# Kernel tuning notes

Hardware: AMD Instinct MI355X
Metric: run time of the kernel (lower is better)

## Reference

```python
import jax, jax.numpy as jnp
import numpy as np

DELTA_V = 0.5
DELTA_D = 1.5
ALPHA = 1.0
BETA = 1.0
GAMMA = 0.001
K = 33  # label ids 0..32; 0 = background (ignored)
EPS = 1e-12


def setup_inputs() -> dict:
    key = jax.random.key(0)
    k1, k2 = jax.random.split(key)
    B, N, E = 8, 65536, 32
    embeddings = jax.random.normal(k1, (B, N, E), dtype=jnp.float32)
    labels = jax.random.randint(k2, (B, N), 0, K)
    return {"embeddings": embeddings, "labels": labels}


def reference(embeddings, labels):
    B, N, E = embeddings.shape
    dt = embeddings.dtype
    seg = (labels + jnp.arange(B)[:, None] * K).reshape(-1)  # (B*N,)

    # segment mean -> per-instance centers (B, K, E)
    sums = jax.ops.segment_sum(embeddings.reshape(B * N, E), seg, num_segments=B * K).reshape(B, K, E)
    counts = jax.ops.segment_sum(jnp.ones((B * N,), dtype=dt), seg, num_segments=B * K).reshape(B, K)
    centers = sums / jnp.maximum(counts, 1.0)[..., None]

    present = counts > 0
    present = present.at[:, 0].set(False)  # drop background label 0
    presf = present.astype(dt)
    n_inst = presf.sum(axis=1)  # (B,)

    # ---- variance term: per-point hinge distance to own center, segment-mean ----
    c_per_point = centers[jnp.arange(B)[:, None], labels]  # (B, N, E) gather
    d2 = ((embeddings - c_per_point) ** 2).sum(-1)
    dist = jnp.sqrt(jnp.maximum(d2, EPS))
    hinge = jnp.where(labels > 0, jnp.maximum(dist - DELTA_V, 0.0), 0.0)
    per_inst_sum = jax.ops.segment_sum(hinge.reshape(-1), seg, num_segments=B * K).reshape(B, K)
    per_inst_mean = per_inst_sum / jnp.maximum(counts, 1.0)
    variance_term = (per_inst_mean * presf).sum(1) / jnp.maximum(n_inst, 1.0)

    # ---- distance term: pairwise hinge between present instance centers ----
    diff2 = ((centers[:, :, None, :] - centers[:, None, :, :]) ** 2).sum(-1)  # (B,K,K)
    upper = jnp.triu(jnp.ones((K, K), dtype=bool), 1)[None]
    pair_valid = present[:, :, None] & present[:, None, :] & upper
    cd = jnp.sqrt(jnp.maximum(jnp.where(pair_valid, diff2, 1.0), EPS))
    pair_hinge = jnp.maximum(2.0 * DELTA_D - cd, 0.0) * pair_valid.astype(dt)
    n_pairs = n_inst * (n_inst - 1.0) * 0.5
    distance_term = pair_hinge.sum((1, 2)) / jnp.maximum(n_pairs, 1.0)

    # ---- regularization: mean L2 norm of present centers ----
    c_norm = jnp.sqrt(jnp.maximum((centers ** 2).sum(-1), EPS))
    reg_term = (c_norm * presf).sum(1) / jnp.maximum(n_inst, 1.0)

    per_batch = ALPHA * variance_term + BETA * distance_term + GAMMA * reg_term
    per_batch = jnp.where(n_inst > 0, per_batch, 0.0)
    return per_batch.sum() / B
```

## Files before the change

### kernel.cpp

```cpp
#include <hip/hip_runtime.h>
#include <math.h>

#define KC 33
#define ED 32
#define KE (KC * ED)
#define PAD 33

#define BPB_A 64
#define TPA 128
#define NSLOT 8
#define BPB_H 128
#define TPH 256


__global__ void k_zero(float* __restrict__ ws, int n, float* __restrict__ out) {
    int i = blockIdx.x * blockDim.x + threadIdx.x;
    if (i < n) ws[i] = 0.f;
    if (i == 0) out[0] = 0.f;
}

__global__ __launch_bounds__(256) void k_hist(const int* __restrict__ lab,
                                              float* __restrict__ counts, int N) {
    __shared__ float h[4 * KC];
    int t = threadIdx.x;
    int w = t >> 6;
    if (t < 4 * KC) h[t] = 0.f;
    __syncthreads();
    int b   = blockIdx.x >> 5;
    int blk = blockIdx.x & 31;
    const int4* l4 = (const int4*)(lab + (size_t)b * N + (size_t)blk * 2048);
    int4 a = l4[t];
    int4 c = l4[t + 256];
    float* hw = &h[w * KC];
    atomicAdd(&hw[a.x], 1.f); atomicAdd(&hw[a.y], 1.f);
    atomicAdd(&hw[a.z], 1.f); atomicAdd(&hw[a.w], 1.f);
    atomicAdd(&hw[c.x], 1.f); atomicAdd(&hw[c.y], 1.f);
    atomicAdd(&hw[c.z], 1.f); atomicAdd(&hw[c.w], 1.f);
    __syncthreads();
    if (t < KC)
        atomicAdd(&counts[b * KC + t], h[t] + h[KC + t] + h[2 * KC + t] + h[3 * KC + t]);
}

__global__ __launch_bounds__(256) void k_accum(const float* __restrict__ emb,
                                               const int* __restrict__ lab,
                                               float* __restrict__ sums, int N) {
    __shared__ float s_tile[TPA * PAD];
    __shared__ float s_priv[NSLOT * KE];
    __shared__ int   s_lab[TPA];
    int t = threadIdx.x;
    for (int i = t; i < NSLOT * KE; i += 256) s_priv[i] = 0.f;

    int b     = blockIdx.x / BPB_A;
    int blk   = blockIdx.x % BPB_A;
    int chunk = N / BPB_A;
    int e     = t & 31;
    int slot  = t >> 5;
    size_t pbase = (size_t)b * N + (size_t)blk * chunk;
    const int NT = chunk / TPA;

    const float4* g4 = (const float4*)(emb + pbase * ED);
    float4 r0 = g4[t], r1 = g4[t + 256], r2 = g4[t + 512], r3 = g4[t + 768];
    int rl = 0;
    if (t < TPA) rl = lab[pbase + t];
    __syncthreads();

    for (int tb = 0; tb < NT; tb++) {
        {
            int f, p, m;
            f = t;        p = f >> 3; m = (f & 7) * 4;
            { float* d = &s_tile[PAD * p + m]; d[0]=r0.x; d[1]=r0.y; d[2]=r0.z; d[3]=r0.w; }
            f = t + 256;  p = f >> 3; m = (f & 7) * 4;
            { float* d = &s_tile[PAD * p + m]; d[0]=r1.x; d[1]=r1.y; d[2]=r1.z; d[3]=r1.w; }
            f = t + 512;  p = f >> 3; m = (f & 7) * 4;
            { float* d = &s_tile[PAD * p + m]; d[0]=r2.x; d[1]=r2.y; d[2]=r2.z; d[3]=r2.w; }
            f = t + 768;  p = f >> 3; m = (f & 7) * 4;
            { float* d = &s_tile[PAD * p + m]; d[0]=r3.x; d[1]=r3.y; d[2]=r3.z; d[3]=r3.w; }
        }
        if (t < TPA) s_lab[t] = rl;
        __syncthreads();

        if (tb + 1 < NT) {
            const float4* gn = (const float4*)(emb + (pbase + (size_t)(tb + 1) * TPA) * ED);
            r0 = gn[t]; r1 = gn[t + 256]; r2 = gn[t + 512]; r3 = gn[t + 768];
            if (t < TPA) rl = lab[pbase + (size_t)(tb + 1) * TPA + t];
        }

        float* priv = &s_priv[slot * KE];
#pragma unroll
        for (int st = 0; st < TPA / NSLOT; st++) {
            int pt = st * NSLOT + slot;
            float x = s_tile[pt * PAD + e];
            int   k = s_lab[pt];
            priv[k * ED + e] += x;
        }
        __syncthreads();
    }

    for (int i = t; i < KE; i += 256) {
        float v = 0.f;
#pragma unroll
        for (int s = 0; s < NSLOT; s++) v += s_priv[s * KE + i];
        atomicAdd(&sums[(size_t)b * KE + i], v);
    }
}

__global__ __launch_bounds__(256) void k_hinge(const float* __restrict__ emb,
                                               const int* __restrict__ lab,
                                               const float* __restrict__ sums,
                                               const float* __restrict__ counts,
                                               float* __restrict__ var, int N) {
    __shared__ float s_tile[TPH * PAD];
    __shared__ float s_ctr[KC * PAD];
    __shared__ float s_cnt[KC];
    __shared__ float s_inv[KC];
    __shared__ int   s_lab[TPH];
    __shared__ float s_red[4];
    int t     = threadIdx.x;
    int b     = blockIdx.x / BPB_H;
    int blk   = blockIdx.x % BPB_H;
    int chunk = N / BPB_H;
    size_t pbase = (size_t)b * N + (size_t)blk * chunk;
    const int NT = chunk / TPH;

    const float4* g4 = (const float4*)(emb + pbase * ED);
    float4 r0 = g4[t],        r1 = g4[t + 256],  r2 = g4[t + 512],  r3 = g4[t + 768];
    float4 r4 = g4[t + 1024], r5 = g4[t + 1280], r6 = g4[t + 1536], r7 = g4[t + 1792];
    int rl = lab[pbase + t];

    if (t < KC) {
        float c = counts[b * KC + t];
        s_cnt[t] = fmaxf(c, 1.f);
        s_inv[t] = (t > 0 && c > 0.f) ? 1.f / fmaxf(c, 1.f) : 0.f;
    }
    __syncthreads();
    for (int i = t; i < KE; i += 256) {
        int k = i >> 5, e = i & 31;
        s_ctr[k * PAD + e] = sums[(size_t)b * KE + i] / s_cnt[k];
    }

    float hs = 0.f;
    for (int tb = 0; tb < NT; tb++) {
        {
            int f, p, m;
            f = t;         p = f >> 3; m = (f & 7) * 4;
            { float* d = &s_tile[PAD * p + m]; d[0]=r0.x; d[1]=r0.y; d[2]=r0.z; d[3]=r0.w; }
            f = t + 256;   p = f >> 3; m = (f & 7) * 4;
            { float* d = &s_tile[PAD * p + m]; d[0]=r1.x; d[1]=r1.y; d[2]=r1.z; d[3]=r1.w; }
            f = t + 512;   p = f >> 3; m = (f & 7) * 4;
            { float* d = &s_tile[PAD * p + m]; d[0]=r2.x; d[1]=r2.y; d[2]=r2.z; d[3]=r2.w; }
            f = t + 768;   p = f >> 3; m = (f & 7) * 4;
            { float* d = &s_tile[PAD * p + m]; d[0]=r3.x; d[1]=r3.y; d[2]=r3.z; d[3]=r3.w; }
            f = t + 1024;  p = f >> 3; m = (f & 7) * 4;
            { float* d = &s_tile[PAD * p + m]; d[0]=r4.x; d[1]=r4.y; d[2]=r4.z; d[3]=r4.w; }
            f = t + 1280;  p = f >> 3; m = (f & 7) * 4;
            { float* d = &s_tile[PAD * p + m]; d[0]=r5.x; d[1]=r5.y; d[2]=r5.z; d[3]=r5.w; }
            f = t + 1536;  p = f >> 3; m = (f & 7) * 4;
            { float* d = &s_tile[PAD * p + m]; d[0]=r6.x; d[1]=r6.y; d[2]=r6.z; d[3]=r6.w; }
            f = t + 1792;  p = f >> 3; m = (f & 7) * 4;
            { float* d = &s_tile[PAD * p + m]; d[0]=r7.x; d[1]=r7.y; d[2]=r7.z; d[3]=r7.w; }
        }
        s_lab[t] = rl;
        __syncthreads();

        if (tb + 1 < NT) {
            const float4* gn = (const float4*)(emb + (pbase + (size_t)(tb + 1) * TPH) * ED);
            r0 = gn[t];        r1 = gn[t + 256];  r2 = gn[t + 512];  r3 = gn[t + 768];
            r4 = gn[t + 1024]; r5 = gn[t + 1280]; r6 = gn[t + 1536]; r7 = gn[t + 1792];
            rl = lab[pbase + (size_t)(tb + 1) * TPH + t];
        }

        int   k  = s_lab[t];
        float iv = s_inv[k];
        const float* xr = &s_tile[t * PAD];
        const float* cr = &s_ctr[k * PAD];
        float d2 = 0.f;
#pragma unroll
        for (int j = 0; j < ED; j++) {
            float d = xr[j] - cr[j];
            d2 = fmaf(d, d, d2);
        }
        float dist = sqrtf(fmaxf(d2, 1e-12f));
        hs += fmaxf(dist - 0.5f, 0.f) * iv;
        __syncthreads();
    }

    hs += __shfl_xor(hs, 1);  hs += __shfl_xor(hs, 2);  hs += __shfl_xor(hs, 4);
    hs += __shfl_xor(hs, 8);  hs += __shfl_xor(hs, 16); hs += __shfl_xor(hs, 32);
    if ((t & 63) == 0) s_red[t >> 6] = hs;
    __syncthreads();
    if (t == 0)
        atomicAdd(&var[b], s_red[0] + s_red[1] + s_red[2] + s_red[3]);
}

__global__ __launch_bounds__(256) void k_final(const float* __restrict__ sums,
                                               const float* __restrict__ counts,
                                               const float* __restrict__ var,
                                               float* __restrict__ out, int B) {
    __shared__ float s_ctr[KE];
    __shared__ float s_cnt[KC];
    __shared__ float s_reg[KC];
    __shared__ int   s_prs[KC];
    __shared__ float s_red[256];
    int b = blockIdx.x;
    int t = threadIdx.x;

    if (t < KC) {
        float c = counts[b * KC + t];
        s_cnt[t] = fmaxf(c, 1.f);
        s_prs[t] = (t > 0 && c > 0.f) ? 1 : 0;
    }
    __syncthreads();
    for (int i = t; i < KE; i += 256)
        s_ctr[i] = sums[(size_t)b * KE + i] / s_cnt[i >> 5];
    __syncthreads();
    if (t < KC) {
        float n2 = 0.f;
        for (int e2 = 0; e2 < ED; e2++) { float c = s_ctr[t * ED + e2]; n2 += c * c; }
        s_reg[t] = s_prs[t] ? sqrtf(fmaxf(n2, 1e-12f)) : 0.f;
    }
    __syncthreads();

    float psum = 0.f;
    for (int q = t; q < KC * KC; q += 256) {
        int i = q / KC, j = q % KC;
        if (i < j && s_prs[i] && s_prs[j]) {
            float d2 = 0.f;
            for (int e2 = 0; e2 < ED; e2++) {
                float d = s_ctr[i * ED + e2] - s_ctr[j * ED + e2];
                d2 += d * d;
            }
            float cd = sqrtf(fmaxf(d2, 1e-12f));
            psum += fmaxf(3.0f - cd, 0.f);
        }
    }
    s_red[t] = psum;
    __syncthreads();
    for (int s = 128; s > 0; s >>= 1) {
        if (t < s) s_red[t] += s_red[t + s];
        __syncthreads();
    }

    if (t == 0) {
        float reg = 0.f; int n = 0;
        for (int k = 0; k < KC; k++) { reg += s_reg[k]; n += s_prs[k]; }
        float nf = (float)n;
        float variance_term = var[b] / fmaxf(nf, 1.f);
        float npairs = nf * (nf - 1.f) * 0.5f;
        float distance_term = s_red[0] / fmaxf(npairs, 1.f);
        float reg_term = reg / fmaxf(nf, 1.f);
        float pb = variance_term + distance_term + 0.001f * reg_term;
        if (n == 0) pb = 0.f;
        atomicAdd(out, pb / (float)B);
    }
}

extern "C" void kernel_launch(void* const* d_in, const int* in_sizes, int n_in,
                              void* d_out, int out_size, void* d_ws, size_t ws_size,
                              hipStream_t stream) {
    const float* emb = (const float*)d_in[0];
    const int*   lab = (const int*)d_in[1];
    float* out = (float*)d_out;

    const int B = 8;
    const int N = in_sizes[1] / B;

    float* sums   = (float*)d_ws;
    float* counts = sums + (size_t)B * KE;
    float* var    = counts + (size_t)B * KC;

    int zn = B * KE + B * KC + B;
    k_zero<<<(zn + 255) / 256, 256, 0, stream>>>(sums, zn, out);
    k_hist<<<B * 32, 256, 0, stream>>>(lab, counts, N);
    k_accum<<<B * BPB_A, 256, 0, stream>>>(emb, lab, sums, N);
    k_hinge<<<B * BPB_H, 256, 0, stream>>>(emb, lab, sums, counts, var, N);
    k_final<<<B, 256, 0, stream>>>(sums, counts, var, out, B);
}
```

Measured before the change: 134.1 us.

## Fuse histogram, accumulate, hinge and final kernels into one persistent kernel with grid barriers

Merges the histogram, segment-sum, hinge and final reduction into a single 512-block kernel that uses software grid barriers between phases. The histogram is computed inside the accumulate loop, and each block prefetches its first hinge tile into registers before the barrier so that tile load overlaps the wait. The aim is to remove launch gaps and the separate label pass. The block split for the hinge phase changes from 128 to 64 blocks per batch, which halves that phase's parallelism. The spin barrier relies on all 512 blocks being co-resident, and a deadlock is possible otherwise.

After: 270.0 us. 2.01x slower.

```diff
diff --git a/kernel.cpp b/kernel.cpp
--- a/kernel.cpp
+++ b/kernel.cpp
@@ -5,252 +5,251 @@
 #define ED 32
 #define KE (KC * ED)
 #define PAD 33
-
-#define BPB_A 64
+#define NBLK 512
+#define BPB 64
 #define TPA 128
 #define NSLOT 8
-#define BPB_H 128
 #define TPH 256
 
 
-__global__ void k_zero(float* __restrict__ ws, int n, float* __restrict__ out) {
+__global__ void k_init(float* __restrict__ ws, int nf, int* __restrict__ bar,
+                       float* __restrict__ out) {
     int i = blockIdx.x * blockDim.x + threadIdx.x;
-    if (i < n) ws[i] = 0.f;
+    if (i < nf) ws[i] = 0.f;
+    if (i < 8) bar[i] = 0;
     if (i == 0) out[0] = 0.f;
 }
 
-__global__ __launch_bounds__(256) void k_hist(const int* __restrict__ lab,
-                                              float* __restrict__ counts, int N) {
-    __shared__ float h[4 * KC];
-    int t = threadIdx.x;
-    int w = t >> 6;
-    if (t < 4 * KC) h[t] = 0.f;
+__device__ __forceinline__ void grid_barrier(int* cnt, int* flag) {
+    __threadfence();
     __syncthreads();
-    int b   = blockIdx.x >> 5;
-    int blk = blockIdx.x & 31;
-    const int4* l4 = (const int4*)(lab + (size_t)b * N + (size_t)blk * 2048);
-    int4 a = l4[t];
-    int4 c = l4[t + 256];
-    float* hw = &h[w * KC];
-    atomicAdd(&hw[a.x], 1.f); atomicAdd(&hw[a.y], 1.f);
-    atomicAdd(&hw[a.z], 1.f); atomicAdd(&hw[a.w], 1.f);
-    atomicAdd(&hw[c.x], 1.f); atomicAdd(&hw[c.y], 1.f);
-    atomicAdd(&hw[c.z], 1.f); atomicAdd(&hw[c.w], 1.f);
+    if (threadIdx.x == 0) {
+        int old = __hip_atomic_fetch_add(cnt, 1, __ATOMIC_ACQ_REL, __HIP_MEMORY_SCOPE_AGENT);
+        if (old == NBLK - 1) {
+            __hip_atomic_store(flag, 1, __ATOMIC_RELEASE, __HIP_MEMORY_SCOPE_AGENT);
+        } else {
+            while (__hip_atomic_load(flag, __ATOMIC_RELAXED, __HIP_MEMORY_SCOPE_AGENT) == 0)
+                __builtin_amdgcn_s_sleep(8);
+        }
+    }
     __syncthreads();
-    if (t < KC)
-        atomicAdd(&counts[b * KC + t], h[t] + h[KC + t] + h[2 * KC + t] + h[3 * KC + t]);
-}
-
-__global__ __launch_bounds__(256) void k_accum(const float* __restrict__ emb,
+    __builtin_amdgcn_fence(__ATOMIC_ACQUIRE, "agent");
+}
+
+__global__ __launch_bounds__(256) void k_fused(const float* __restrict__ emb,
                                                const int* __restrict__ lab,
-                                               float* __restrict__ sums, int N) {
-    __shared__ float s_tile[TPA * PAD];
-    __shared__ float s_priv[NSLOT * KE];
-    __shared__ int   s_lab[TPA];
-    int t = threadIdx.x;
-    for (int i = t; i < NSLOT * KE; i += 256) s_priv[i] = 0.f;
-
-    int b     = blockIdx.x / BPB_A;
-    int blk   = blockIdx.x % BPB_A;
-    int chunk = N / BPB_A;
-    int e     = t & 31;
-    int slot  = t >> 5;
+                                               float* __restrict__ sums,
+                                               float* __restrict__ counts,
+                                               float* __restrict__ var,
+                                               int* __restrict__ bar,
+                                               float* __restrict__ out,
+                                               int N) {
+    __shared__ __align__(16) float smem[12840];
+    int t     = threadIdx.x;
+    int b     = blockIdx.x / BPB;
+    int blk   = blockIdx.x % BPB;
+    int chunk = N / BPB;
     size_t pbase = (size_t)b * N + (size_t)blk * chunk;
-    const int NT = chunk / TPA;
-
-    const float4* g4 = (const float4*)(emb + pbase * ED);
-    float4 r0 = g4[t], r1 = g4[t + 256], r2 = g4[t + 512], r3 = g4[t + 768];
-    int rl = 0;
-    if (t < TPA) rl = lab[pbase + t];
-    __syncthreads();
-
-    for (int tb = 0; tb < NT; tb++) {
-        {
-            int f, p, m;
-            f = t;        p = f >> 3; m = (f & 7) * 4;
-            { float* d = &s_tile[PAD * p + m]; d[0]=r0.x; d[1]=r0.y; d[2]=r0.z; d[3]=r0.w; }
-            f = t + 256;  p = f >> 3; m = (f & 7) * 4;
-            { float* d = &s_tile[PAD * p + m]; d[0]=r1.x; d[1]=r1.y; d[2]=r1.z; d[3]=r1.w; }
-            f = t + 512;  p = f >> 3; m = (f & 7) * 4;
-            { float* d = &s_tile[PAD * p + m]; d[0]=r2.x; d[1]=r2.y; d[2]=r2.z; d[3]=r2.w; }
-            f = t + 768;  p = f >> 3; m = (f & 7) * 4;
-            { float* d = &s_tile[PAD * p + m]; d[0]=r3.x; d[1]=r3.y; d[2]=r3.z; d[3]=r3.w; }
-        }
-        if (t < TPA) s_lab[t] = rl;
-        __syncthreads();
-
-        if (tb + 1 < NT) {
-            const float4* gn = (const float4*)(emb + (pbase + (size_t)(tb + 1) * TPA) * ED);
-            r0 = gn[t]; r1 = gn[t + 256]; r2 = gn[t + 512]; r3 = gn[t + 768];
-            if (t < TPA) rl = lab[pbase + (size_t)(tb + 1) * TPA + t];
-        }
-
-        float* priv = &s_priv[slot * KE];
+
+    {
+        float* s_tile = smem;
+        float* s_priv = smem + 4224;
+        int*   s_lab  = (int*)(smem + 12672);
+        float* s_hist = smem + 12800;
+        for (int i = t; i < NSLOT * KE; i += 256) s_priv[i] = 0.f;
+        if (t < KC) s_hist[t] = 0.f;
+        int e = t & 31, slot = t >> 5;
+        const int NT = chunk / TPA;
+
+        const float4* g4 = (const float4*)(emb + pbase * ED);
+        float4 r0 = g4[t], r1 = g4[t + 256], r2 = g4[t + 512], r3 = g4[t + 768];
+        int rl = (t < TPA) ? lab[pbase + t] : 0;
+        __syncthreads();
+
+        for (int tb = 0; tb < NT; tb++) {
+            {
+                int f, p, m;
+                f = t;        p = f >> 3; m = (f & 7) * 4;
+                { float* d = &s_tile[PAD * p + m]; d[0]=r0.x; d[1]=r0.y; d[2]=r0.z; d[3]=r0.w; }
+                f = t + 256;  p = f >> 3; m = (f & 7) * 4;
+                { float* d = &s_tile[PAD * p + m]; d[0]=r1.x; d[1]=r1.y; d[2]=r1.z; d[3]=r1.w; }
+                f = t + 512;  p = f >> 3; m = (f & 7) * 4;
+                { float* d = &s_tile[PAD * p + m]; d[0]=r2.x; d[1]=r2.y; d[2]=r2.z; d[3]=r2.w; }
+                f = t + 768;  p = f >> 3; m = (f & 7) * 4;
+                { float* d = &s_tile[PAD * p + m]; d[0]=r3.x; d[1]=r3.y; d[2]=r3.z; d[3]=r3.w; }
+            }
+            if (t < TPA) s_lab[t] = rl;
+            __syncthreads();
+
+            if (t < TPA) atomicAdd(&s_hist[s_lab[t]], 1.f);
+
+            if (tb + 1 < NT) {
+                const float4* gn = (const float4*)(emb + (pbase + (size_t)(tb + 1) * TPA) * ED);
+                r0 = gn[t]; r1 = gn[t + 256]; r2 = gn[t + 512]; r3 = gn[t + 768];
+                if (t < TPA) rl = lab[pbase + (size_t)(tb + 1) * TPA + t];
+            }
+
+            float* priv = &s_priv[slot * KE];
 #pragma unroll
-        for (int st = 0; st < TPA / NSLOT; st++) {
-            int pt = st * NSLOT + slot;
-            float x = s_tile[pt * PAD + e];
-            int   k = s_lab[pt];
-            priv[k * ED + e] += x;
-        }
-        __syncthreads();
-    }
-
-    for (int i = t; i < KE; i += 256) {
-        float v = 0.f;
+            for (int st = 0; st < TPA / NSLOT; st++) {
+                int pt = st * NSLOT + slot;
+                float x = s_tile[pt * PAD + e];
+                int   k = s_lab[pt];
+                priv[k * ED + e] += x;
+            }
+            __syncthreads();
+        }
+
+        for (int i = t; i < KE; i += 256) {
+            float v = 0.f;
 #pragma unroll
-        for (int s = 0; s < NSLOT; s++) v += s_priv[s * KE + i];
-        atomicAdd(&sums[(size_t)b * KE + i], v);
-    }
-}
-
-__global__ __launch_bounds__(256) void k_hinge(const float* __restrict__ emb,
-                                               const int* __restrict__ lab,
-                                               const float* __restrict__ sums,
-                                               const float* __restrict__ counts,
-                                               float* __restrict__ var, int N) {
-    __shared__ float s_tile[TPH * PAD];
-    __shared__ float s_ctr[KC * PAD];
-    __shared__ float s_cnt[KC];
-    __shared__ float s_inv[KC];
-    __shared__ int   s_lab[TPH];
-    __shared__ float s_red[4];
-    int t     = threadIdx.x;
-    int b     = blockIdx.x / BPB_H;
-    int blk   = blockIdx.x % BPB_H;
-    int chunk = N / BPB_H;
-    size_t pbase = (size_t)b * N + (size_t)blk * chunk;
-    const int NT = chunk / TPH;
-
-    const float4* g4 = (const float4*)(emb + pbase * ED);
-    float4 r0 = g4[t],        r1 = g4[t + 256],  r2 = g4[t + 512],  r3 = g4[t + 768];
-    float4 r4 = g4[t + 1024], r5 = g4[t + 1280], r6 = g4[t + 1536], r7 = g4[t + 1792];
-    int rl = lab[pbase + t];
-
-    if (t < KC) {
-        float c = counts[b * KC + t];
-        s_cnt[t] = fmaxf(c, 1.f);
-        s_inv[t] = (t > 0 && c > 0.f) ? 1.f / fmaxf(c, 1.f) : 0.f;
-    }
-    __syncthreads();
-    for (int i = t; i < KE; i += 256) {
-        int k = i >> 5, e = i & 31;
-        s_ctr[k * PAD + e] = sums[(size_t)b * KE + i] / s_cnt[k];
-    }
-
-    float hs = 0.f;
-    for (int tb = 0; tb < NT; tb++) {
-        {
-            int f, p, m;
-            f = t;         p = f >> 3; m = (f & 7) * 4;
-            { float* d = &s_tile[PAD * p + m]; d[0]=r0.x; d[1]=r0.y; d[2]=r0.z; d[3]=r0.w; }
-            f = t + 256;   p = f >> 3; m = (f & 7) * 4;
-            { float* d = &s_tile[PAD * p + m]; d[0]=r1.x; d[1]=r1.y; d[2]=r1.z; d[3]=r1.w; }
-            f = t + 512;   p = f >> 3; m = (f & 7) * 4;
-            { float* d = &s_tile[PAD * p + m]; d[0]=r2.x; d[1]=r2.y; d[2]=r2.z; d[3]=r2.w; }
-            f = t + 768;   p = f >> 3; m = (f & 7) * 4;
-            { float* d = &s_tile[PAD * p + m]; d[0]=r3.x; d[1]=r3.y; d[2]=r3.z; d[3]=r3.w; }
-            f = t + 1024;  p = f >> 3; m = (f & 7) * 4;
-            { float* d = &s_tile[PAD * p + m]; d[0]=r4.x; d[1]=r4.y; d[2]=r4.z; d[3]=r4.w; }
-            f = t + 1280;  p = f >> 3; m = (f & 7) * 4;
-            { float* d = &s_tile[PAD * p + m]; d[0]=r5.x; d[1]=r5.y; d[2]=r5.z; d[3]=r5.w; }
-            f = t + 1536;  p = f >> 3; m = (f & 7) * 4;
-            { float* d = &s_tile[PAD * p + m]; d[0]=r6.x; d[1]=r6.y; d[2]=r6.z; d[3]=r6.w; }
-            f = t + 1792;  p = f >> 3; m = (f & 7) * 4;
-            { float* d = &s_tile[PAD * p + m]; d[0]=r7.x; d[1]=r7.y; d[2]=r7.z; d[3]=r7.w; }
-        }
-        s_lab[t] = rl;
-        __syncthreads();
-
-        if (tb + 1 < NT) {
-            const float4* gn = (const float4*)(emb + (pbase + (size_t)(tb + 1) * TPH) * ED);
-            r0 = gn[t];        r1 = gn[t + 256];  r2 = gn[t + 512];  r3 = gn[t + 768];
-            r4 = gn[t + 1024]; r5 = gn[t + 1280]; r6 = gn[t + 1536]; r7 = gn[t + 1792];
-            rl = lab[pbase + (size_t)(tb + 1) * TPH + t];
-        }
-
-        int   k  = s_lab[t];
-        float iv = s_inv[k];
-        const float* xr = &s_tile[t * PAD];
-        const float* cr = &s_ctr[k * PAD];
-        float d2 = 0.f;
+            for (int s = 0; s < NSLOT; s++) v += s_priv[s * KE + i];
+            atomicAdd(&sums[(size_t)b * KE + i], v);
+        }
+        if (t < KC) atomicAdd(&counts[b * KC + t], s_hist[t]);
+    }
+
+    float4 q0, q1, q2, q3, q4, q5, q6, q7; int ql;
+    {
+        const float4* g4 = (const float4*)(emb + pbase * ED);
+        q0 = g4[t];        q1 = g4[t + 256];  q2 = g4[t + 512];  q3 = g4[t + 768];
+        q4 = g4[t + 1024]; q5 = g4[t + 1280]; q6 = g4[t + 1536]; q7 = g4[t + 1792];
+        ql = lab[pbase + t];
+    }
+
+    grid_barrier(bar + 0, bar + 1);
+
+    {
+        float* s_tile = smem;
+        float* s_ctr  = smem + 8448;
+        float* s_inv  = smem + 9537;
+        int*   s_lab  = (int*)(smem + 9570);
+        float* s_red  = smem + 9826;
+        float* s_cnt  = smem + 9830;
+        if (t < KC) {
+            float c = counts[b * KC + t];
+            s_cnt[t] = fmaxf(c, 1.f);
+            s_inv[t] = (t > 0 && c > 0.f) ? 1.f / fmaxf(c, 1.f) : 0.f;
+        }
+        __syncthreads();
+        for (int i = t; i < KE; i += 256) {
+            int k = i >> 5, e2 = i & 31;
+            s_ctr[k * PAD + e2] = sums[(size_t)b * KE + i] / s_cnt[k];
+        }
+
+        float hs = 0.f;
+        const int NT2 = chunk / TPH;
+        for (int tb = 0; tb < NT2; tb++) {
+            {
+                int f, p, m;
+                f = t;         p = f >> 3; m = (f & 7) * 4;
+                { float* d = &s_tile[PAD * p + m]; d[0]=q0.x; d[1]=q0.y; d[2]=q0.z; d[3]=q0.w; }
+                f = t + 256;   p = f >> 3; m = (f & 7) * 4;
+                { float* d = &s_tile[PAD * p + m]; d[0]=q1.x; d[1]=q1.y; d[2]=q1.z; d[3]=q1.w; }
+                f = t + 512;   p = f >> 3; m = (f & 7) * 4;
+                { float* d = &s_tile[PAD * p + m]; d[0]=q2.x; d[1]=q2.y; d[2]=q2.z; d[3]=q2.w; }
+                f = t + 768;   p = f >> 3; m = (f & 7) * 4;
+                { float* d = &s_tile[PAD * p + m]; d[0]=q3.x; d[1]=q3.y; d[2]=q3.z; d[3]=q3.w; }
+                f = t + 1024;  p = f >> 3; m = (f & 7) * 4;
+                { float* d = &s_tile[PAD * p + m]; d[0]=q4.x; d[1]=q4.y; d[2]=q4.z; d[3]=q4.w; }
+                f = t + 1280;  p = f >> 3; m = (f & 7) * 4;
+                { float* d = &s_tile[PAD * p + m]; d[0]=q5.x; d[1]=q5.y; d[2]=q5.z; d[3]=q5.w; }
+                f = t + 1536;  p = f >> 3; m = (f & 7) * 4;
+                { float* d = &s_tile[PAD * p + m]; d[0]=q6.x; d[1]=q6.y; d[2]=q6.z; d[3]=q6.w; }
+                f = t + 1792;  p = f >> 3; m = (f & 7) * 4;
+                { float* d = &s_tile[PAD * p + m]; d[0]=q7.x; d[1]=q7.y; d[2]=q7.z; d[3]=q7.w; }
+            }
+            s_lab[t] = ql;
+            __syncthreads();
+
+            if (tb + 1 < NT2) {
+                const float4* gn = (const float4*)(emb + (pbase + (size_t)(tb + 1) * TPH) * ED);
+                q0 = gn[t];        q1 = gn[t + 256];  q2 = gn[t + 512];  q3 = gn[t + 768];
+                q4 = gn[t + 1024]; q5 = gn[t + 1280]; q6 = gn[t + 1536]; q7 = gn[t + 1792];
+                ql = lab[pbase + (size_t)(tb + 1) * TPH + t];
+            }
+
+            int   k  = s_lab[t];
+            float iv = s_inv[k];
+            const float* xr = &s_tile[t * PAD];
+            const float* cr = &s_ctr[k * PAD];
+            float d2 = 0.f;
 #pragma unroll
-        for (int j = 0; j < ED; j++) {
-            float d = xr[j] - cr[j];
-            d2 = fmaf(d, d, d2);
-        }
-        float dist = sqrtf(fmaxf(d2, 1e-12f));
-        hs += fmaxf(dist - 0.5f, 0.f) * iv;
-        __syncthreads();
-    }
-
-    hs += __shfl_xor(hs, 1);  hs += __shfl_xor(hs, 2);  hs += __shfl_xor(hs, 4);
-    hs += __shfl_xor(hs, 8);  hs += __shfl_xor(hs, 16); hs += __shfl_xor(hs, 32);
-    if ((t & 63) == 0) s_red[t >> 6] = hs;
-    __syncthreads();
-    if (t == 0)
-        atomicAdd(&var[b], s_red[0] + s_red[1] + s_red[2] + s_red[3]);
-}
-
-__global__ __launch_bounds__(256) void k_final(const float* __restrict__ sums,
-                                               const float* __restrict__ counts,
-                                               const float* __restrict__ var,
-                                               float* __restrict__ out, int B) {
-    __shared__ float s_ctr[KE];
-    __shared__ float s_cnt[KC];
-    __shared__ float s_reg[KC];
-    __shared__ int   s_prs[KC];
-    __shared__ float s_red[256];
-    int b = blockIdx.x;
-    int t = threadIdx.x;
-
-    if (t < KC) {
-        float c = counts[b * KC + t];
-        s_cnt[t] = fmaxf(c, 1.f);
-        s_prs[t] = (t > 0 && c > 0.f) ? 1 : 0;
-    }
-    __syncthreads();
-    for (int i = t; i < KE; i += 256)
-        s_ctr[i] = sums[(size_t)b * KE + i] / s_cnt[i >> 5];
-    __syncthreads();
-    if (t < KC) {
-        float n2 = 0.f;
-        for (int e2 = 0; e2 < ED; e2++) { float c = s_ctr[t * ED + e2]; n2 += c * c; }
-        s_reg[t] = s_prs[t] ? sqrtf(fmaxf(n2, 1e-12f)) : 0.f;
-    }
-    __syncthreads();
-
-    float psum = 0.f;
-    for (int q = t; q < KC * KC; q += 256) {
-        int i = q / KC, j = q % KC;
-        if (i < j && s_prs[i] && s_prs[j]) {
-            float d2 = 0.f;
-            for (int e2 = 0; e2 < ED; e2++) {
-                float d = s_ctr[i * ED + e2] - s_ctr[j * ED + e2];
-                d2 += d * d;
-            }
-            float cd = sqrtf(fmaxf(d2, 1e-12f));
-            psum += fmaxf(3.0f - cd, 0.f);
-        }
-    }
-    s_red[t] = psum;
-    __syncthreads();
-    for (int s = 128; s > 0; s >>= 1) {
-        if (t < s) s_red[t] += s_red[t + s];
-        __syncthreads();
-    }
-
-    if (t == 0) {
-        float reg = 0.f; int n = 0;
-        for (int k = 0; k < KC; k++) { reg += s_reg[k]; n += s_prs[k]; }
-        float nf = (float)n;
-        float variance_term = var[b] / fmaxf(nf, 1.f);
-        float npairs = nf * (nf - 1.f) * 0.5f;
-        float distance_term = s_red[0] / fmaxf(npairs, 1.f);
-        float reg_term = reg / fmaxf(nf, 1.f);
-        float pb = variance_term + distance_term + 0.001f * reg_term;
-        if (n == 0) pb = 0.f;
-        atomicAdd(out, pb / (float)B);
+            for (int j = 0; j < ED; j++) {
+                float d = xr[j] - cr[j];
+                d2 = fmaf(d, d, d2);
+            }
+            float dist = sqrtf(fmaxf(d2, 1e-12f));
+            hs += fmaxf(dist - 0.5f, 0.f) * iv;
+            __syncthreads();
+        }
+
+        hs += __shfl_xor(hs, 1);  hs += __shfl_xor(hs, 2);  hs += __shfl_xor(hs, 4);
+        hs += __shfl_xor(hs, 8);  hs += __shfl_xor(hs, 16); hs += __shfl_xor(hs, 32);
+        if ((t & 63) == 0) s_red[t >> 6] = hs;
+        __syncthreads();
+        if (t == 0)
+            atomicAdd(&var[b], s_red[0] + s_red[1] + s_red[2] + s_red[3]);
+    }
+
+    grid_barrier(bar + 2, bar + 3);
+
+    if (blockIdx.x < 8) {
+        int fb = blockIdx.x;
+        float* s_ctr = smem;
+        float* s_cnt = smem + 1056;
+        float* s_reg = smem + 1089;
+        int*   s_prs = (int*)(smem + 1122);
+        float* s_red = smem + 1155;
+
+        if (t < KC) {
+            float c = counts[fb * KC + t];
+            s_cnt[t] = fmaxf(c, 1.f);
+            s_prs[t] = (t > 0 && c > 0.f) ? 1 : 0;
+        }
+        __syncthreads();
+        for (int i = t; i < KE; i += 256)
+            s_ctr[i] = sums[(size_t)fb * KE + i] / s_cnt[i >> 5];
+        __syncthreads();
+        if (t < KC) {
+            float n2 = 0.f;
+            for (int e2 = 0; e2 < ED; e2++) { float c = s_ctr[t * ED + e2]; n2 += c * c; }
+            s_reg[t] = s_prs[t] ? sqrtf(fmaxf(n2, 1e-12f)) : 0.f;
+        }
+        __syncthreads();
+
+        float psum = 0.f;
+        for (int q = t; q < KC * KC; q += 256) {
+            int i = q / KC, j = q % KC;
+            if (i < j && s_prs[i] && s_prs[j]) {
+                float d2 = 0.f;
+                for (int e2 = 0; e2 < ED; e2++) {
+                    float d = s_ctr[i * ED + e2] - s_ctr[j * ED + e2];
+                    d2 += d * d;
+                }
+                float cd = sqrtf(fmaxf(d2, 1e-12f));
+                psum += fmaxf(3.0f - cd, 0.f);
+            }
+        }
+        s_red[t] = psum;
+        __syncthreads();
+        for (int s = 128; s > 0; s >>= 1) {
+            if (t < s) s_red[t] += s_red[t + s];
+            __syncthreads();
+        }
+
+        if (t == 0) {
+            float reg = 0.f; int n = 0;
+            for (int k = 0; k < KC; k++) { reg += s_reg[k]; n += s_prs[k]; }
+            float nf = (float)n;
+            float variance_term = var[fb] / fmaxf(nf, 1.f);
+            float npairs = nf * (nf - 1.f) * 0.5f;
+            float distance_term = s_red[0] / fmaxf(npairs, 1.f);
+            float reg_term = reg / fmaxf(nf, 1.f);
+            float pb = variance_term + distance_term + 0.001f * reg_term;
+            if (n == 0) pb = 0.f;
+            atomicAdd(out, pb * 0.125f);
+        }
     }
 }
 
@@ -267,11 +266,9 @@
     float* sums   = (float*)d_ws;
     float* counts = sums + (size_t)B * KE;
     float* var    = counts + (size_t)B * KC;
-
-    int zn = B * KE + B * KC + B;
-    k_zero<<<(zn + 255) / 256, 256, 0, stream>>>(sums, zn, out);
-    k_hist<<<B * 32, 256, 0, stream>>>(lab, counts, N);
-    k_accum<<<B * BPB_A, 256, 0, stream>>>(emb, lab, sums, N);
-    k_hinge<<<B * BPB_H, 256, 0, stream>>>(emb, lab, sums, counts, var, N);
-    k_final<<<B, 256, 0, stream>>>(sums, counts, var, out, B);
-}
+    int*   bar    = (int*)(var + B);
+
+    int nf = B * KE + B * KC + B;
+    k_init<<<(nf + 255) / 256, 256, 0, stream>>>(sums, nf, bar, out);
+    k_fused<<<NBLK, 256, 0, stream>>>(emb, lab, sums, counts, var, bar, out, N);
+}
```
